# Kernel tuning notes

Measured on AMD Instinct MI355X. Metric: run time of the kernel, lower is better.

Reference implementation:

```python
import jax, jax.numpy as jnp
import numpy as np

N, E, D, H, Dh, B = 100000, 600000, 128, 8, 16, 20
NEG_SLOPE = 0.2  # DGL GATConv default

def setup_inputs() -> dict:
    key = jax.random.key(0)
    ks = jax.random.split(key, 10)
    stdv = 1.0 / np.sqrt(D)
    return {
        "input": jax.random.normal(ks[0], (N, D), jnp.float32),
        "h0": jax.random.normal(ks[1], (N, D), jnp.float32),
        "src": jax.random.randint(ks[2], (E,), 0, N),
        "dst": jax.random.randint(ks[3], (E,), 0, N),
        "cums": jnp.arange(0, N + 1, N // B, dtype=jnp.int32),  # B equal subgraphs
        "l": 2,
        "lamda": jnp.float32(0.5),
        "alpha": jnp.float32(0.1),
        "W_fc": jax.random.normal(ks[4], (D, H * Dh), jnp.float32) * 0.05,
        "attn_l": jax.random.normal(ks[5], (H, Dh), jnp.float32) * 0.05,
        "attn_r": jax.random.normal(ks[6], (H, Dh), jnp.float32) * 0.05,
        "gat_bias": jnp.zeros((H * Dh,), jnp.float32),
        "W_comb": jax.random.uniform(ks[7], (2 * D, D), jnp.float32, -stdv, stdv),
        "gamma": jnp.ones((1, D), jnp.float32),
        "beta": jnp.zeros((1, D), jnp.float32),
    }

def reference(input, h0, src, dst, cums, l, lamda, alpha, W_fc, attn_l, attn_r,
              gat_bias, W_comb, gamma, beta):
    n = input.shape[0]
    # --- DGL GATConv: fc -> per-edge scores -> edge softmax by dst -> scatter ---
    h = (input @ W_fc).reshape(n, H, Dh)                    # (N,H,Dh)
    el = (h * attn_l).sum(-1)                               # (N,H)
    er = (h * attn_r).sum(-1)                               # (N,H)
    e = jax.nn.leaky_relu(el[src] + er[dst], NEG_SLOPE)     # (E,H)
    m = jax.ops.segment_max(e, dst, num_segments=n)         # (N,H)
    ex = jnp.exp(e - m[dst])
    denom = jax.ops.segment_sum(ex, dst, num_segments=n)
    a = ex / denom[dst]                                     # (E,H)
    msg = a[:, :, None] * h[src]                            # (E,H,Dh)
    rst = jax.ops.segment_sum(msg, dst, num_segments=n)
    x = (rst + gat_bias.reshape(1, H, Dh)).reshape(n, H * Dh)
    # --- GCNII combine ---
    theta = jnp.minimum(1.0, jnp.log(lamda / l + 1.0))
    support = jnp.concatenate([x, h0], axis=1)              # (N,2D)
    r = (1.0 - alpha) * x + alpha * h0
    x = theta * (support @ W_comb) + (1.0 - theta) * r
    x = x + input
    # --- per-subgraph GraphNorm (unbiased std, like torch.std) ---
    sid = jnp.searchsorted(cums, jnp.arange(n), side="right") - 1  # (N,)
    nb = cums.shape[0] - 1
    cnt = jax.ops.segment_sum(jnp.ones((n,), x.dtype), sid, num_segments=nb)
    mean = jax.ops.segment_sum(x, sid, num_segments=nb) / cnt[:, None]
    c = x - mean[sid]
    var = jax.ops.segment_sum(c * c, sid, num_segments=nb) / (cnt - 1.0)[:, None]
    std = jnp.sqrt(var)
    return gamma * (c / (std[sid] + 1e-5)) + beta
```

## Files before the change

kernel.cpp:

```cpp
#include <hip/hip_runtime.h>
#include <hip/hip_bf16.h>

#define NEG_SLOPE 0.2f
#define STATS_SPLIT 50

typedef short bf16x8 __attribute__((ext_vector_type(8)));
typedef float f32x4 __attribute__((ext_vector_type(4)));

__device__ __forceinline__ unsigned short f2bf(float f) {
    unsigned int u = __float_as_uint(f);
    unsigned int r = (u + 0x7fffu + ((u >> 16) & 1u)) >> 16;
    return (unsigned short)r;
}
__device__ __forceinline__ float bf2f(unsigned short h) {
    return __uint_as_float(((unsigned int)h) << 16);
}

__global__ __launch_bounds__(256) void prep_kernel(
    const float* __restrict__ W_fc, const float* __restrict__ attn_l,
    const float* __restrict__ attn_r, const float* __restrict__ W_comb,
    const float* __restrict__ gat_bias,
    const int* __restrict__ l_p, const float* __restrict__ lamda_p,
    const float* __restrict__ alpha_p,
    unsigned short* __restrict__ Wt_fc, unsigned short* __restrict__ Wt_cb,
    float* __restrict__ bvec)
{
    const float alpha = alpha_p[0];
    const float theta = fminf(1.0f, logf(lamda_p[0] / (float)l_p[0] + 1.0f));
    const float c1 = (1.f - theta) * (1.f - alpha);
    const float c2 = (1.f - theta) * alpha;

    const int t = blockIdx.x * 256 + threadIdx.x;
    const int stride = gridDim.x * 256;
    for (int i = t; i < 128 * 128; i += stride) {
        const int c = i >> 7, k = i & 127;
        Wt_fc[c * 128 + k] = f2bf(W_fc[k * 128 + c]);
    }
    for (int i = t; i < 8 * 128; i += stride) {
        const int hd = i >> 7, k = i & 127;
        float sl = 0.f, sr = 0.f;
        for (int d = 0; d < 16; ++d) {
            const float w = W_fc[k * 128 + hd * 16 + d];
            sl += w * attn_l[hd * 16 + d];
            sr += w * attn_r[hd * 16 + d];
        }
        Wt_fc[(128 + hd) * 128 + k] = f2bf(sl);
        Wt_fc[(136 + hd) * 128 + k] = f2bf(sr);
    }
    for (int i = t; i < 128 * 256; i += stride) {
        const int c = i >> 8, k = i & 255;
        float w = theta * W_comb[k * 128 + c];
        if (k == c) w += c1;
        if (k == c + 128) w += c2;
        Wt_cb[c * 256 + k] = f2bf(w);
    }
    for (int c = t; c < 128; c += stride) {
        float s = c1 * gat_bias[c];
        for (int k = 0; k < 128; ++k)
            s += theta * gat_bias[k] * W_comb[k * 128 + c];
        bvec[c] = s;
    }
}

__global__ __launch_bounds__(256) void fc_gemm_kernel(
    const float* __restrict__ A, const unsigned short* __restrict__ Wt,
    unsigned short* __restrict__ h, float* __restrict__ el,
    float* __restrict__ er, int n)
{
    __shared__ unsigned short As[64][36];
    __shared__ unsigned short Bs[144][36];
    const int tid = threadIdx.x;
    const int wave = tid >> 6;
    const int lane = tid & 63;
    const int m16 = lane & 15;
    const int kg = lane >> 4;
    const int rowBase = blockIdx.x * 64;

    f32x4 acc[9];
#pragma unroll
    for (int t = 0; t < 9; ++t) acc[t] = (f32x4){0.f, 0.f, 0.f, 0.f};

    const int rS = tid >> 2;
    const int pS = tid & 3;

    for (int ci = 0; ci < 4; ++ci) {
        const int kc = ci * 32;
        if (ci) __syncthreads();
        {
            int row = rowBase + rS;
            if (row >= n) row = n - 1;
            const float4 v0 = *(const float4*)&A[(long long)row * 128 + kc + pS * 8];
            const float4 v1 = *(const float4*)&A[(long long)row * 128 + kc + pS * 8 + 4];
            bf16x8 pk;
            pk[0] = (short)f2bf(v0.x); pk[1] = (short)f2bf(v0.y);
            pk[2] = (short)f2bf(v0.z); pk[3] = (short)f2bf(v0.w);
            pk[4] = (short)f2bf(v1.x); pk[5] = (short)f2bf(v1.y);
            pk[6] = (short)f2bf(v1.z); pk[7] = (short)f2bf(v1.w);
            *(bf16x8*)&As[rS][pS * 8] = pk;
        }
        for (int i = tid; i < 576; i += 256) {
            const int r = i >> 2, p = i & 3;
            *(bf16x8*)&Bs[r][p * 8] =
                *(const bf16x8*)&Wt[r * 128 + kc + p * 8];
        }
        __syncthreads();

        const bf16x8 afrag = *(const bf16x8*)&As[wave * 16 + m16][kg * 8];
#pragma unroll
        for (int t = 0; t < 9; ++t) {
            const bf16x8 bfrag = *(const bf16x8*)&Bs[t * 16 + m16][kg * 8];
            acc[t] = __builtin_amdgcn_mfma_f32_16x16x32_bf16(afrag, bfrag, acc[t], 0, 0, 0);
        }
    }

    const int r0 = rowBase + wave * 16 + kg * 4;
#pragma unroll
    for (int t = 0; t < 8; ++t) {
#pragma unroll
        for (int j = 0; j < 4; ++j) {
            const int row = r0 + j;
            if (row < n)
                h[(long long)row * 128 + t * 16 + m16] = f2bf(acc[t][j]);
        }
    }
#pragma unroll
    for (int j = 0; j < 4; ++j) {
        const int row = r0 + j;
        if (row < n) {
            const float v = acc[8][j];
            if (m16 < 8) el[(long long)row * 8 + m16] = v;
            else         er[(long long)row * 8 + (m16 - 8)] = v;
        }
    }
}

__global__ __launch_bounds__(256) void hist_kernel(
    const int* __restrict__ dst, int* __restrict__ deg, int E)
{
    const int i = blockIdx.x * 256 + threadIdx.x;
    if (i < E) atomicAdd(&deg[dst[i]], 1);
}

__global__ __launch_bounds__(256) void scan1_kernel(
    const int* __restrict__ deg, int* __restrict__ row,
    int* __restrict__ blockSums, int n)
{
    __shared__ int sdata[256];
    const int t = threadIdx.x;
    const int base = blockIdx.x * 1024 + t * 4;
    int v[4];
    int tot = 0;
#pragma unroll
    for (int j = 0; j < 4; ++j) {
        v[j] = (base + j < n) ? deg[base + j] : 0;
        tot += v[j];
    }
    sdata[t] = tot;
    __syncthreads();
    for (int off = 1; off < 256; off <<= 1) {
        const int x = (t >= off) ? sdata[t - off] : 0;
        __syncthreads();
        sdata[t] += x;
        __syncthreads();
    }
    if (t == 255) blockSums[blockIdx.x] = sdata[255];
    int run = sdata[t] - tot;
#pragma unroll
    for (int j = 0; j < 4; ++j) {
        if (base + j < n) row[base + j] = run;
        run += v[j];
    }
}

__global__ __launch_bounds__(128) void scan2_kernel(
    int* __restrict__ blockSums, int nb)
{
    __shared__ int sdata[128];
    const int t = threadIdx.x;
    const int v = (t < nb) ? blockSums[t] : 0;
    sdata[t] = v;
    __syncthreads();
    for (int off = 1; off < 128; off <<= 1) {
        const int x = (t >= off) ? sdata[t - off] : 0;
        __syncthreads();
        sdata[t] += x;
        __syncthreads();
    }
    if (t < nb) blockSums[t] = sdata[t] - v;
}

__global__ __launch_bounds__(256) void scan3_kernel(
    int* __restrict__ row, int* __restrict__ cursor,
    const int* __restrict__ blockSums, int n, int E)
{
    const int i = blockIdx.x * 256 + threadIdx.x;
    if (i == 0) row[n] = E;
    if (i >= n) return;
    const int r = row[i] + blockSums[i >> 10];
    row[i] = r;
    cursor[i] = r;
}

__global__ __launch_bounds__(256) void scatter_kernel(
    const int* __restrict__ src, const int* __restrict__ dst,
    int* __restrict__ cursor, int* __restrict__ srcs, int E)
{
    const int i = blockIdx.x * 256 + threadIdx.x;
    if (i >= E) return;
    const int pos = atomicAdd(&cursor[dst[i]], 1);
    srcs[pos] = src[i];
}

__global__ __launch_bounds__(256) void aggregate_kernel(
    const float* __restrict__ el, const float* __restrict__ er,
    const unsigned short* __restrict__ h, const int* __restrict__ row,
    const int* __restrict__ srcs, unsigned short* __restrict__ rst, int n)
{
    const int d = blockIdx.x * 4 + (threadIdx.x >> 6);
    const int lane = threadIdx.x & 63;
    if (d >= n) return;
    const int start = row[d], end = row[d + 1];
    const int hd = lane >> 3;
    const float erd = er[(long long)d * 8 + hd];

    float acc0 = 0.f, acc1 = 0.f, den = 0.f;
    for (int p = start; p < end; p += 64) {
        const int cnt = min(64, end - p);
        const int sv = srcs[p + (lane < cnt ? lane : cnt - 1)];
        int j = 0;
        for (; j + 1 < cnt; j += 2) {
            const int s0 = __shfl(sv, j);
            const int s1 = __shfl(sv, j + 1);
            const float g0 = el[(long long)s0 * 8 + hd];
            const float g1 = el[(long long)s1 * 8 + hd];
            const unsigned int u0 = *(const unsigned int*)&h[(long long)s0 * 128 + lane * 2];
            const unsigned int u1 = *(const unsigned int*)&h[(long long)s1 * 128 + lane * 2];
            float e0 = g0 + erd; e0 = e0 >= 0.f ? e0 : NEG_SLOPE * e0;
            float e1 = g1 + erd; e1 = e1 >= 0.f ? e1 : NEG_SLOPE * e1;
            const float w0 = __expf(e0);
            const float w1 = __expf(e1);
            den += w0 + w1;
            acc0 += w0 * __uint_as_float(u0 << 16)
                  + w1 * __uint_as_float(u1 << 16);
            acc1 += w0 * __uint_as_float(u0 & 0xffff0000u)
                  + w1 * __uint_as_float(u1 & 0xffff0000u);
        }
        if (j < cnt) {
            const int s0 = __shfl(sv, j);
            const unsigned int u0 = *(const unsigned int*)&h[(long long)s0 * 128 + lane * 2];
            float e0 = el[(long long)s0 * 8 + hd] + erd;
            e0 = e0 >= 0.f ? e0 : NEG_SLOPE * e0;
            const float w0 = __expf(e0);
            den += w0;
            acc0 += w0 * __uint_as_float(u0 << 16);
            acc1 += w0 * __uint_as_float(u0 & 0xffff0000u);
        }
    }
    ushort2 o;
    if (end > start) {
        const float inv = 1.f / den;
        o.x = f2bf(acc0 * inv);
        o.y = f2bf(acc1 * inv);
    } else {
        o.x = 0; o.y = 0;
    }
    *(ushort2*)&rst[(long long)d * 128 + lane * 2] = o;
}

__global__ __launch_bounds__(256) void combine_gemm_kernel(
    const unsigned short* __restrict__ rst, const float* __restrict__ h0,
    const float* __restrict__ input, const unsigned short* __restrict__ Wt,
    const float* __restrict__ bvec, float* __restrict__ x, int n)
{
    __shared__ unsigned short As[2][64][36];
    __shared__ unsigned short Bs[2][128][36];
    const int tid = threadIdx.x;
    const int wave = tid >> 6;
    const int lane = tid & 63;
    const int m16 = lane & 15;
    const int kg = lane >> 4;
    const int rowBase = blockIdx.x * 64;

    f32x4 acc[8];
#pragma unroll
    for (int t = 0; t < 8; ++t) acc[t] = (f32x4){0.f, 0.f, 0.f, 0.f};

    const int rS = tid >> 2;
    const int pS = tid & 3;
    const int rB = tid >> 1;
    const int p0 = (tid & 1) * 2;

    float4 va0, va1;
    bf16x8 vr, vb0, vb1;
    int arow = rowBase + rS;
    if (arow >= n) arow = n - 1;
    const long long aoff = (long long)arow * 128;

#define CB_LOAD(ci)                                                           \
    {                                                                         \
        const int kc = (ci) * 32;                                             \
        const int koff = kc & 127;                                            \
        if ((ci) < 4) {                                                       \
            vr = *(const bf16x8*)&rst[aoff + koff + pS * 8];                  \
        } else {                                                              \
            va0 = *(const float4*)&h0[aoff + koff + pS * 8];                  \
            va1 = *(const float4*)&h0[aoff + koff + pS * 8 + 4];              \
        }                                                                     \
        vb0 = *(const bf16x8*)&Wt[rB * 256 + kc + p0 * 8];                    \
        vb1 = *(const bf16x8*)&Wt[rB * 256 + kc + p0 * 8 + 8];                \
    }

#define CB_WRITE(buf, ci)                                                     \
    {                                                                         \
        if ((ci) < 4) {                                                       \
            *(bf16x8*)&As[buf][rS][pS * 8] = vr;                              \
        } else {                                                              \
            bf16x8 pk;                                                        \
            pk[0] = (short)f2bf(va0.x); pk[1] = (short)f2bf(va0.y);           \
            pk[2] = (short)f2bf(va0.z); pk[3] = (short)f2bf(va0.w);           \
            pk[4] = (short)f2bf(va1.x); pk[5] = (short)f2bf(va1.y);           \
            pk[6] = (short)f2bf(va1.z); pk[7] = (short)f2bf(va1.w);           \
            *(bf16x8*)&As[buf][rS][pS * 8] = pk;                              \
        }                                                                     \
        *(bf16x8*)&Bs[buf][rB][p0 * 8] = vb0;                                 \
        *(bf16x8*)&Bs[buf][rB][p0 * 8 + 8] = vb1;                             \
    }

    CB_LOAD(0)
    CB_WRITE(0, 0)
    __syncthreads();

#pragma unroll
    for (int ci = 0; ci < 8; ++ci) {
        const int cur = ci & 1;
        if (ci < 7) CB_LOAD(ci + 1)
        const bf16x8 afrag = *(const bf16x8*)&As[cur][wave * 16 + m16][kg * 8];
#pragma unroll
        for (int t = 0; t < 8; ++t) {
            const bf16x8 bfrag = *(const bf16x8*)&Bs[cur][t * 16 + m16][kg * 8];
            acc[t] = __builtin_amdgcn_mfma_f32_16x16x32_bf16(afrag, bfrag, acc[t], 0, 0, 0);
        }
        if (ci < 7) {
            CB_WRITE(cur ^ 1, ci + 1)
            __syncthreads();
        }
    }
#undef CB_LOAD
#undef CB_WRITE

    const int r0 = rowBase + wave * 16 + kg * 4;
#pragma unroll
    for (int t = 0; t < 8; ++t) {
        const int col = t * 16 + m16;
        const float bv = bvec[col];
#pragma unroll
        for (int j = 0; j < 4; ++j) {
            const int row = r0 + j;
            if (row < n) {
                const long long off = (long long)row * 128 + col;
                x[off] = acc[t][j] + bv + input[off];
            }
        }
    }
}

__global__ __launch_bounds__(128) void stats_kernel(
    const float* __restrict__ x, const int* __restrict__ cums,
    float* __restrict__ sums, float* __restrict__ sumsq)
{
    const int b = blockIdx.x / STATS_SPLIT;
    const int part = blockIdx.x % STATS_SPLIT;
    const int tid = threadIdx.x;
    const int start = cums[b], end = cums[b + 1];
    float s = 0.f, s2 = 0.f;
    for (int node = start + part; node < end; node += STATS_SPLIT) {
        const float v = x[(long long)node * 128 + tid];
        s += v;
        s2 += v * v;
    }
    atomicAdd(&sums[b * 128 + tid], s);
    atomicAdd(&sumsq[b * 128 + tid], s2);
}

__global__ __launch_bounds__(128) void finalize_stats_kernel(
    const int* __restrict__ cums, float* __restrict__ sums,
    float* __restrict__ sumsq)
{
    const int b = blockIdx.x;
    const int tid = threadIdx.x;
    const float cnt = (float)(cums[b + 1] - cums[b]);
    const float s = sums[b * 128 + tid];
    const float s2 = sumsq[b * 128 + tid];
    const float mean = s / cnt;
    float var = (s2 - s * mean) / (cnt - 1.f);
    var = fmaxf(var, 0.f);
    sums[b * 128 + tid] = mean;
    sumsq[b * 128 + tid] = 1.f / (sqrtf(var) + 1e-5f);
}

__global__ __launch_bounds__(256) void norm_kernel(
    const float* __restrict__ x, const float* __restrict__ mean,
    const float* __restrict__ istd, const int* __restrict__ cums, int nb,
    const float* __restrict__ gamma, const float* __restrict__ beta,
    float* __restrict__ out, int n)
{
    const long long gid = (long long)blockIdx.x * 256 + threadIdx.x;
    const int node = (int)(gid >> 5);
    if (node >= n) return;
    const int f4 = (int)(gid & 31);
    int lo = 0, hi = nb;
    while (hi - lo > 1) {
        const int mid = (lo + hi) >> 1;
        if (cums[mid] <= node) lo = mid; else hi = mid;
    }
    const float4 m = *(const float4*)&mean[lo * 128 + f4 * 4];
    const float4 is = *(const float4*)&istd[lo * 128 + f4 * 4];
    const float4 g = *(const float4*)&gamma[f4 * 4];
    const float4 bt = *(const float4*)&beta[f4 * 4];
    const float4 v = *(const float4*)&x[(long long)node * 128 + f4 * 4];
    float4 o;
    o.x = g.x * ((v.x - m.x) * is.x) + bt.x;
    o.y = g.y * ((v.y - m.y) * is.y) + bt.y;
    o.z = g.z * ((v.z - m.z) * is.z) + bt.z;
    o.w = g.w * ((v.w - m.w) * is.w) + bt.w;
    *(float4*)&out[(long long)node * 128 + f4 * 4] = o;
}

extern "C" void kernel_launch(void* const* d_in, const int* in_sizes, int n_in,
                              void* d_out, int out_size, void* d_ws, size_t ws_size,
                              hipStream_t stream) {
    const float* input   = (const float*)d_in[0];
    const float* h0      = (const float*)d_in[1];
    const int*   src     = (const int*)d_in[2];
    const int*   dst     = (const int*)d_in[3];
    const int*   cums    = (const int*)d_in[4];
    const int*   l_p     = (const int*)d_in[5];
    const float* lamda_p = (const float*)d_in[6];
    const float* alpha_p = (const float*)d_in[7];
    const float* W_fc    = (const float*)d_in[8];
    const float* attn_l  = (const float*)d_in[9];
    const float* attn_r  = (const float*)d_in[10];
    const float* gat_bias= (const float*)d_in[11];
    const float* W_comb  = (const float*)d_in[12];
    const float* gamma   = (const float*)d_in[13];
    const float* beta    = (const float*)d_in[14];

    const int n  = in_sizes[0] / 128;
    const int E  = in_sizes[2];
    const int nb = in_sizes[4] - 1;
    float* out = (float*)d_out;

    char* ws = (char*)d_ws;
    size_t o = 0;
#define ALLOC(ptr, type, count)                                              \
    type* ptr = (type*)(ws + o); o = (o + (size_t)(count) * sizeof(type) + 15) & ~(size_t)15;
    ALLOC(h,        unsigned short, (size_t)n * 128)
    ALLOC(el,       float,          (size_t)n * 8)
    ALLOC(er,       float,          (size_t)n * 8)
    ALLOC(rst,      unsigned short, (size_t)n * 128)
    ALLOC(sums,     float,          (size_t)nb * 128)
    ALLOC(sumsq,    float,          (size_t)nb * 128)
    ALLOC(deg,      int,            (size_t)n)
    ALLOC(row_ptr,  int,            (size_t)n + 1)
    ALLOC(cursor,   int,            (size_t)n)
    ALLOC(blockSums,int,            128)
    ALLOC(srcs,     int,            (size_t)E)
    ALLOC(Wt_fc,    unsigned short, 144 * 128)
    ALLOC(Wt_cb,    unsigned short, 128 * 256)
    ALLOC(bvec,     float,          128)
#undef ALLOC

    hipMemsetAsync(deg, 0, (size_t)n * 4, stream);
    hipMemsetAsync(sums, 0, (size_t)nb * 128 * 4, stream);
    hipMemsetAsync(sumsq, 0, (size_t)nb * 128 * 4, stream);

    prep_kernel<<<64, 256, 0, stream>>>(
        W_fc, attn_l, attn_r, W_comb, gat_bias, l_p, lamda_p, alpha_p,
        Wt_fc, Wt_cb, bvec);

    hist_kernel<<<(E + 255) / 256, 256, 0, stream>>>(dst, deg, E);
    const int nblk1 = (n + 1023) / 1024;
    scan1_kernel<<<nblk1, 256, 0, stream>>>(deg, row_ptr, blockSums, n);
    scan2_kernel<<<1, 128, 0, stream>>>(blockSums, nblk1);
    scan3_kernel<<<(n + 255) / 256, 256, 0, stream>>>(row_ptr, cursor, blockSums, n, E);
    scatter_kernel<<<(E + 255) / 256, 256, 0, stream>>>(src, dst, cursor, srcs, E);

    const int gemm_grid = (n + 63) / 64;
    fc_gemm_kernel<<<gemm_grid, 256, 0, stream>>>(input, Wt_fc, h, el, er, n);

    aggregate_kernel<<<(n + 3) / 4, 256, 0, stream>>>(
        el, er, h, row_ptr, srcs, rst, n);

    combine_gemm_kernel<<<gemm_grid, 256, 0, stream>>>(
        rst, h0, input, Wt_cb, bvec, out, n);

    stats_kernel<<<nb * STATS_SPLIT, 128, 0, stream>>>(out, cums, sums, sumsq);
    finalize_stats_kernel<<<nb, 128, 0, stream>>>(cums, sums, sumsq);

    const long long norm_threads = (long long)n * 32;
    norm_kernel<<<(int)((norm_threads + 255) / 256), 256, 0, stream>>>(
        out, sums, sumsq, cums, nb, gamma, beta, out, n);
}
```

Measured before the change: 246.5 us.

## Fuse GraphNorm statistics into combine GEMM and keep A fragments in registers

The per-subgraph sum and sum-of-squares reduction moves into the combine GEMM epilogue, using wave shuffles, shared-memory atomics and global atomics. This removes the separate stats kernel and its re-read of the output. Both GEMMs now load their A operand straight into registers per wave instead of staging it through shared memory, and the fc GEMM double-buffers its weight tiles. The cost is more registers per thread. The stats path also assumes a 64-row block spans at most two subgraphs.

```diff
diff --git a/kernel.cpp b/kernel.cpp
--- a/kernel.cpp
+++ b/kernel.cpp
@@ -2,7 +2,6 @@
 #include <hip/hip_bf16.h>
 
 #define NEG_SLOPE 0.2f
-#define STATS_SPLIT 50
 
 typedef short bf16x8 __attribute__((ext_vector_type(8)));
 typedef float f32x4 __attribute__((ext_vector_type(4)));
@@ -67,8 +66,7 @@
     unsigned short* __restrict__ h, float* __restrict__ el,
     float* __restrict__ er, int n)
 {
-    __shared__ unsigned short As[64][36];
-    __shared__ unsigned short Bs[144][36];
+    __shared__ unsigned short Bs[2][144][36];
     const int tid = threadIdx.x;
     const int wave = tid >> 6;
     const int lane = tid & 63;
@@ -76,42 +74,72 @@
     const int kg = lane >> 4;
     const int rowBase = blockIdx.x * 64;
 
+    int arow = rowBase + wave * 16 + m16;
+    if (arow >= n) arow = n - 1;
+    const long long aoff = (long long)arow * 128;
+    bf16x8 af[4];
+#pragma unroll
+    for (int ci = 0; ci < 4; ++ci) {
+        const float4 v0 = *(const float4*)&A[aoff + ci * 32 + kg * 8];
+        const float4 v1 = *(const float4*)&A[aoff + ci * 32 + kg * 8 + 4];
+        bf16x8 pk;
+        pk[0] = (short)f2bf(v0.x); pk[1] = (short)f2bf(v0.y);
+        pk[2] = (short)f2bf(v0.z); pk[3] = (short)f2bf(v0.w);
+        pk[4] = (short)f2bf(v1.x); pk[5] = (short)f2bf(v1.y);
+        pk[6] = (short)f2bf(v1.z); pk[7] = (short)f2bf(v1.w);
+        af[ci] = pk;
+    }
+
+    const int rB = tid >> 1;
+    const int p0 = (tid & 1) * 2;
+    const bool hasU2 = tid < 32;
+    const int rB2 = 128 + (tid >> 1);
+
+    bf16x8 vb0, vb1, w0, w1;
+#define FC_BLOAD(ci)                                                         \
+    {                                                                        \
+        const int kc = (ci) * 32;                                            \
+        vb0 = *(const bf16x8*)&Wt[rB * 128 + kc + p0 * 8];                   \
+        vb1 = *(const bf16x8*)&Wt[rB * 128 + kc + p0 * 8 + 8];               \
+        if (hasU2) {                                                         \
+            w0 = *(const bf16x8*)&Wt[rB2 * 128 + kc + p0 * 8];               \
+            w1 = *(const bf16x8*)&Wt[rB2 * 128 + kc + p0 * 8 + 8];           \
+        }                                                                    \
+    }
+#define FC_BWRITE(buf)                                                       \
+    {                                                                        \
+        *(bf16x8*)&Bs[buf][rB][p0 * 8] = vb0;                                \
+        *(bf16x8*)&Bs[buf][rB][p0 * 8 + 8] = vb1;                            \
+        if (hasU2) {                                                         \
+            *(bf16x8*)&Bs[buf][rB2][p0 * 8] = w0;                            \
+            *(bf16x8*)&Bs[buf][rB2][p0 * 8 + 8] = w1;                        \
+        }                                                                    \
+    }
+
     f32x4 acc[9];
 #pragma unroll
     for (int t = 0; t < 9; ++t) acc[t] = (f32x4){0.f, 0.f, 0.f, 0.f};
 
-    const int rS = tid >> 2;
-    const int pS = tid & 3;
-
+    FC_BLOAD(0)
+    FC_BWRITE(0)
+    __syncthreads();
+
+#pragma unroll
     for (int ci = 0; ci < 4; ++ci) {
-        const int kc = ci * 32;
-        if (ci) __syncthreads();
-        {
-            int row = rowBase + rS;
-            if (row >= n) row = n - 1;
-            const float4 v0 = *(const float4*)&A[(long long)row * 128 + kc + pS * 8];
-            const float4 v1 = *(const float4*)&A[(long long)row * 128 + kc + pS * 8 + 4];
-            bf16x8 pk;
-            pk[0] = (short)f2bf(v0.x); pk[1] = (short)f2bf(v0.y);
-            pk[2] = (short)f2bf(v0.z); pk[3] = (short)f2bf(v0.w);
-            pk[4] = (short)f2bf(v1.x); pk[5] = (short)f2bf(v1.y);
-            pk[6] = (short)f2bf(v1.z); pk[7] = (short)f2bf(v1.w);
-            *(bf16x8*)&As[rS][pS * 8] = pk;
-        }
-        for (int i = tid; i < 576; i += 256) {
-            const int r = i >> 2, p = i & 3;
-            *(bf16x8*)&Bs[r][p * 8] =
-                *(const bf16x8*)&Wt[r * 128 + kc + p * 8];
-        }
-        __syncthreads();
-
-        const bf16x8 afrag = *(const bf16x8*)&As[wave * 16 + m16][kg * 8];
+        const int cur = ci & 1;
+        if (ci < 3) FC_BLOAD(ci + 1)
 #pragma unroll
         for (int t = 0; t < 9; ++t) {
-            const bf16x8 bfrag = *(const bf16x8*)&Bs[t * 16 + m16][kg * 8];
-            acc[t] = __builtin_amdgcn_mfma_f32_16x16x32_bf16(afrag, bfrag, acc[t], 0, 0, 0);
-        }
-    }
+            const bf16x8 bfrag = *(const bf16x8*)&Bs[cur][t * 16 + m16][kg * 8];
+            acc[t] = __builtin_amdgcn_mfma_f32_16x16x32_bf16(af[ci], bfrag, acc[t], 0, 0, 0);
+        }
+        if (ci < 3) {
+            FC_BWRITE(cur ^ 1)
+            __syncthreads();
+        }
+    }
+#undef FC_BLOAD
+#undef FC_BWRITE
 
     const int r0 = rowBase + wave * 16 + kg * 4;
 #pragma unroll
@@ -270,10 +298,12 @@
 __global__ __launch_bounds__(256) void combine_gemm_kernel(
     const unsigned short* __restrict__ rst, const float* __restrict__ h0,
     const float* __restrict__ input, const unsigned short* __restrict__ Wt,
-    const float* __restrict__ bvec, float* __restrict__ x, int n)
-{
-    __shared__ unsigned short As[2][64][36];
+    const float* __restrict__ bvec, const int* __restrict__ cums, int nb,
+    float* __restrict__ sums, float* __restrict__ sumsq,
+    float* __restrict__ x, int n)
+{
     __shared__ unsigned short Bs[2][128][36];
+    __shared__ float s_sum[128], s_sq[128];
     const int tid = threadIdx.x;
     const int wave = tid >> 6;
     const int lane = tid & 63;
@@ -281,105 +311,103 @@
     const int kg = lane >> 4;
     const int rowBase = blockIdx.x * 64;
 
-    f32x4 acc[8];
-#pragma unroll
-    for (int t = 0; t < 8; ++t) acc[t] = (f32x4){0.f, 0.f, 0.f, 0.f};
-
-    const int rS = tid >> 2;
-    const int pS = tid & 3;
+    if (tid < 128) { s_sum[tid] = 0.f; s_sq[tid] = 0.f; }
+
+    int arow = rowBase + wave * 16 + m16;
+    if (arow >= n) arow = n - 1;
+    const long long aoff = (long long)arow * 128;
+    bf16x8 af[8];
+#pragma unroll
+    for (int ci = 0; ci < 4; ++ci)
+        af[ci] = *(const bf16x8*)&rst[aoff + ci * 32 + kg * 8];
+#pragma unroll
+    for (int ci = 0; ci < 4; ++ci) {
+        const float4 v0 = *(const float4*)&h0[aoff + ci * 32 + kg * 8];
+        const float4 v1 = *(const float4*)&h0[aoff + ci * 32 + kg * 8 + 4];
+        bf16x8 pk;
+        pk[0] = (short)f2bf(v0.x); pk[1] = (short)f2bf(v0.y);
+        pk[2] = (short)f2bf(v0.z); pk[3] = (short)f2bf(v0.w);
+        pk[4] = (short)f2bf(v1.x); pk[5] = (short)f2bf(v1.y);
+        pk[6] = (short)f2bf(v1.z); pk[7] = (short)f2bf(v1.w);
+        af[4 + ci] = pk;
+    }
+
     const int rB = tid >> 1;
     const int p0 = (tid & 1) * 2;
-
-    float4 va0, va1;
-    bf16x8 vr, vb0, vb1;
-    int arow = rowBase + rS;
-    if (arow >= n) arow = n - 1;
-    const long long aoff = (long long)arow * 128;
-
-#define CB_LOAD(ci)                                                           \
-    {                                                                         \
-        const int kc = (ci) * 32;                                             \
-        const int koff = kc & 127;                                            \
-        if ((ci) < 4) {                                                       \
-            vr = *(const bf16x8*)&rst[aoff + koff + pS * 8];                  \
-        } else {                                                              \
-            va0 = *(const float4*)&h0[aoff + koff + pS * 8];                  \
-            va1 = *(const float4*)&h0[aoff + koff + pS * 8 + 4];              \
-        }                                                                     \
-        vb0 = *(const bf16x8*)&Wt[rB * 256 + kc + p0 * 8];                    \
-        vb1 = *(const bf16x8*)&Wt[rB * 256 + kc + p0 * 8 + 8];                \
-    }
-
-#define CB_WRITE(buf, ci)                                                     \
-    {                                                                         \
-        if ((ci) < 4) {                                                       \
-            *(bf16x8*)&As[buf][rS][pS * 8] = vr;                              \
-        } else {                                                              \
-            bf16x8 pk;                                                        \
-            pk[0] = (short)f2bf(va0.x); pk[1] = (short)f2bf(va0.y);           \
-            pk[2] = (short)f2bf(va0.z); pk[3] = (short)f2bf(va0.w);           \
-            pk[4] = (short)f2bf(va1.x); pk[5] = (short)f2bf(va1.y);           \
-            pk[6] = (short)f2bf(va1.z); pk[7] = (short)f2bf(va1.w);           \
-            *(bf16x8*)&As[buf][rS][pS * 8] = pk;                              \
-        }                                                                     \
-        *(bf16x8*)&Bs[buf][rB][p0 * 8] = vb0;                                 \
-        *(bf16x8*)&Bs[buf][rB][p0 * 8 + 8] = vb1;                             \
-    }
-
-    CB_LOAD(0)
-    CB_WRITE(0, 0)
+    bf16x8 vb0, vb1;
+
+    f32x4 acc[8];
+#pragma unroll
+    for (int t = 0; t < 8; ++t) acc[t] = (f32x4){0.f, 0.f, 0.f, 0.f};
+
+    vb0 = *(const bf16x8*)&Wt[rB * 256 + p0 * 8];
+    vb1 = *(const bf16x8*)&Wt[rB * 256 + p0 * 8 + 8];
+    *(bf16x8*)&Bs[0][rB][p0 * 8] = vb0;
+    *(bf16x8*)&Bs[0][rB][p0 * 8 + 8] = vb1;
     __syncthreads();
 
 #pragma unroll
     for (int ci = 0; ci < 8; ++ci) {
         const int cur = ci & 1;
-        if (ci < 7) CB_LOAD(ci + 1)
-        const bf16x8 afrag = *(const bf16x8*)&As[cur][wave * 16 + m16][kg * 8];
+        if (ci < 7) {
+            vb0 = *(const bf16x8*)&Wt[rB * 256 + (ci + 1) * 32 + p0 * 8];
+            vb1 = *(const bf16x8*)&Wt[rB * 256 + (ci + 1) * 32 + p0 * 8 + 8];
+        }
 #pragma unroll
         for (int t = 0; t < 8; ++t) {
             const bf16x8 bfrag = *(const bf16x8*)&Bs[cur][t * 16 + m16][kg * 8];
-            acc[t] = __builtin_amdgcn_mfma_f32_16x16x32_bf16(afrag, bfrag, acc[t], 0, 0, 0);
+            acc[t] = __builtin_amdgcn_mfma_f32_16x16x32_bf16(af[ci], bfrag, acc[t], 0, 0, 0);
         }
         if (ci < 7) {
-            CB_WRITE(cur ^ 1, ci + 1)
+            *(bf16x8*)&Bs[cur ^ 1][rB][p0 * 8] = vb0;
+            *(bf16x8*)&Bs[cur ^ 1][rB][p0 * 8 + 8] = vb1;
             __syncthreads();
         }
     }
-#undef CB_LOAD
-#undef CB_WRITE
+
+    int lo = 0, hi = nb;
+    while (hi - lo > 1) {
+        const int mid = (lo + hi) >> 1;
+        if (cums[mid] <= rowBase) lo = mid; else hi = mid;
+    }
+    const int sid0 = lo;
+    const int bnd = cums[sid0 + 1];
 
     const int r0 = rowBase + wave * 16 + kg * 4;
 #pragma unroll
     for (int t = 0; t < 8; ++t) {
         const int col = t * 16 + m16;
         const float bv = bvec[col];
+        float s0 = 0.f, q0 = 0.f, s1 = 0.f, q1 = 0.f;
 #pragma unroll
         for (int j = 0; j < 4; ++j) {
             const int row = r0 + j;
             if (row < n) {
                 const long long off = (long long)row * 128 + col;
-                x[off] = acc[t][j] + bv + input[off];
+                const float val = acc[t][j] + bv + input[off];
+                x[off] = val;
+                if (row < bnd) { s0 += val; q0 += val * val; }
+                else           { s1 += val; q1 += val * val; }
             }
         }
-    }
-}
-
-__global__ __launch_bounds__(128) void stats_kernel(
-    const float* __restrict__ x, const int* __restrict__ cums,
-    float* __restrict__ sums, float* __restrict__ sumsq)
-{
-    const int b = blockIdx.x / STATS_SPLIT;
-    const int part = blockIdx.x % STATS_SPLIT;
-    const int tid = threadIdx.x;
-    const int start = cums[b], end = cums[b + 1];
-    float s = 0.f, s2 = 0.f;
-    for (int node = start + part; node < end; node += STATS_SPLIT) {
-        const float v = x[(long long)node * 128 + tid];
-        s += v;
-        s2 += v * v;
-    }
-    atomicAdd(&sums[b * 128 + tid], s);
-    atomicAdd(&sumsq[b * 128 + tid], s2);
+        s0 += __shfl_xor(s0, 16, 64); s0 += __shfl_xor(s0, 32, 64);
+        q0 += __shfl_xor(q0, 16, 64); q0 += __shfl_xor(q0, 32, 64);
+        s1 += __shfl_xor(s1, 16, 64); s1 += __shfl_xor(s1, 32, 64);
+        q1 += __shfl_xor(q1, 16, 64); q1 += __shfl_xor(q1, 32, 64);
+        if (kg == 0) {
+            atomicAdd(&s_sum[col], s0);
+            atomicAdd(&s_sq[col], q0);
+            if (s1 != 0.f || q1 != 0.f) {
+                atomicAdd(&sums[(sid0 + 1) * 128 + col], s1);
+                atomicAdd(&sumsq[(sid0 + 1) * 128 + col], q1);
+            }
+        }
+    }
+    __syncthreads();
+    if (tid < 128) {
+        atomicAdd(&sums[sid0 * 128 + tid], s_sum[tid]);
+        atomicAdd(&sumsq[sid0 * 128 + tid], s_sq[tid]);
+    }
 }
 
 __global__ __launch_bounds__(128) void finalize_stats_kernel(
@@ -492,9 +520,8 @@
         el, er, h, row_ptr, srcs, rst, n);
 
     combine_gemm_kernel<<<gemm_grid, 256, 0, stream>>>(
-        rst, h0, input, Wt_cb, bvec, out, n);
-
-    stats_kernel<<<nb * STATS_SPLIT, 128, 0, stream>>>(out, cums, sums, sumsq);
+        rst, h0, input, Wt_cb, bvec, cums, nb, sums, sumsq, out, n);
+
     finalize_stats_kernel<<<nb, 128, 0, stream>>>(cums, sums, sumsq);
 
     const long long norm_threads = (long long)n * 32;
```

Result: faster. 225.8 us (-8.4%).
